# Kernel tuning notes

Measured on AMD Instinct MI355X. Metric: run time of the kernel, lower is better.

Reference implementation:

```python
import jax, jax.numpy as jnp
import numpy as np

B, N, C = 32, 577, 768
H = 12
DH = C // H  # 64
SCALE = DH ** -0.5


def setup_inputs() -> dict:
    key = jax.random.key(0)
    ks = jax.random.split(key, 5)
    x = jax.random.normal(ks[0], (B, N, C), dtype=jnp.float32)
    # Linear params (torch convention: y = x @ W.T + b)
    qkv_w = jax.random.normal(ks[1], (3 * C, C), dtype=jnp.float32) * (C ** -0.5)
    qkv_b = jnp.zeros((3 * C,), dtype=jnp.float32)
    proj_w = jax.random.normal(ks[2], (C, C), dtype=jnp.float32) * (C ** -0.5)
    proj_b = jnp.zeros((C,), dtype=jnp.float32)
    return {"x": x, "qkv_w": qkv_w, "qkv_b": qkv_b, "proj_w": proj_w, "proj_b": proj_b}


def reference(x, qkv_w, qkv_b, proj_w, proj_b):
    b, n, c = x.shape
    qkv = x @ qkv_w.T + qkv_b                       # [B, N, 3C]
    qkv = qkv.reshape(b, n, 3, H, DH).transpose(2, 0, 3, 1, 4)  # [3, B, H, N, DH]
    q, k, v = qkv[0], qkv[1], qkv[2]
    q = q * SCALE
    attn = jnp.einsum('bhnd,bhmd->bhnm', q, k)      # [B, H, N, N]
    # sigmoid -> inverse-sigmoid straight-through rewrite (forward equals logit(sigmoid(attn)))
    sig = jax.nn.sigmoid(attn)
    inv_sig = jnp.log(sig / (1.0 - sig))
    attn_st = attn + jax.lax.stop_gradient(inv_sig - attn)
    p = jax.nn.softmax(attn_st, axis=-1)
    out = jnp.einsum('bhnm,bhmd->bhnd', p, v)       # [B, H, N, DH]
    out = out.transpose(0, 2, 1, 3).reshape(b, n, c)
    return out @ proj_w.T + proj_b
```

## Files before the change

kernel.cpp:

```cpp
#include <hip/hip_runtime.h>

typedef __bf16 bf16;
typedef __attribute__((ext_vector_type(4))) __bf16 bf16x4;
typedef __attribute__((ext_vector_type(8))) __bf16 bf16x8;
typedef __attribute__((ext_vector_type(4))) float f32x4;

#define MFMA_BF16(A_, B_, C_) __builtin_amdgcn_mfma_f32_16x16x32_bf16(A_, B_, C_, 0, 0, 0)

#define BB    32
#define SEQ   577
#define CH    768
#define NH    12
#define DHD   64
#define MROWS (BB * SEQ)
#define NQKV  2304
#define SEQP  584
#define QSCALE 0.1803368801111204f

#define NSTEP 24

__device__ __forceinline__ int xcd_chunk(int bid, int nwg) {
  int q8 = nwg >> 3, r8 = nwg & 7;
  int xcd = bid & 7, sub = bid >> 3;
  return (xcd < r8 ? xcd * (q8 + 1) : r8 * (q8 + 1) + (xcd - r8) * q8) + sub;
}

__device__ __forceinline__ void async_ld16(const bf16* g, bf16* l) {
  __builtin_amdgcn_global_load_lds(
      (const __attribute__((address_space(1))) void*)g,
      (__attribute__((address_space(3))) void*)l, 16, 0, 0);
}

__global__ __launch_bounds__(256) void cvt_bf16(const float* __restrict__ src,
                                                bf16* __restrict__ dst, int n) {
  int idx = (blockIdx.x * 256 + threadIdx.x) * 4;
  if (idx >= n) return;
  float4 v = *(const float4*)(src + idx);
  bf16x4 o = {(bf16)v.x, (bf16)v.y, (bf16)v.z, (bf16)v.w};
  *(bf16x4*)(dst + idx) = o;
}

__global__ __launch_bounds__(256) void pad_v(bf16* __restrict__ vt) {
  int r = blockIdx.x * 256 + threadIdx.x;
  if (r < BB * NH * DHD) {
    bf16* p = vt + (size_t)r * SEQP + SEQ;
#pragma unroll
    for (int i = 0; i < 7; ++i) p[i] = (bf16)0.f;
  }
}

__global__ __launch_bounds__(256, 2)
void gemm_qkv(const bf16* __restrict__ A, const bf16* __restrict__ W,
              const float* __restrict__ bias,
              bf16* __restrict__ qrm, bf16* __restrict__ krm, bf16* __restrict__ vt) {
  __shared__ bf16 As[2][128 * 32];
  __shared__ bf16 Bs[2][128 * 32];
  const int tid = threadIdx.x, lane = tid & 63, wid = tid >> 6;
  const int quad = lane >> 4, r15 = lane & 15;
  const int nbx = (int)gridDim.x;
  const int wg = xcd_chunk((int)blockIdx.y * nbx + (int)blockIdx.x,
                           nbx * (int)gridDim.y);
  const int m0 = (wg / nbx) * 128, n0 = (wg % nbx) * 128;
  const int waveM = wid & 1, waveN = wid >> 1;

  const bf16* aSrc[2];
  const bf16* bSrc[2];
  for (int c = 0; c < 2; ++c) {
    int q = wid * 128 + c * 64 + lane;
    int row = q >> 2;
    int sw = (row ^ (row >> 2)) & 3;
    int kc = (q & 3) ^ sw;
    aSrc[c] = A + (size_t)(m0 + row) * CH + kc * 8;
    bSrc[c] = W + (size_t)(n0 + row) * CH + kc * 8;
  }

  f32x4 acc[4][4];
#pragma unroll
  for (int i = 0; i < 4; ++i)
#pragma unroll
    for (int j = 0; j < 4; ++j) acc[i][j] = (f32x4){0.f, 0.f, 0.f, 0.f};

#define GSTAGE(K0, BUF)                                                   \
  {                                                                       \
    _Pragma("unroll") for (int c = 0; c < 2; ++c) {                       \
      async_ld16(aSrc[c] + (K0), &As[BUF][(wid * 128 + c * 64) * 8]);     \
      async_ld16(bSrc[c] + (K0), &Bs[BUF][(wid * 128 + c * 64) * 8]);     \
    }                                                                     \
  }

#define GCOMPUTE(BUF)                                                     \
  {                                                                       \
    bf16x8 af[4], bfr[4];                                                 \
    _Pragma("unroll") for (int s = 0; s < 4; ++s) {                       \
      int rowA = waveM * 64 + s * 16 + r15;                               \
      int ca = quad ^ ((rowA ^ (rowA >> 2)) & 3);                         \
      af[s] = *(const bf16x8*)(&As[BUF][rowA * 32 + ca * 8]);             \
      int rowB = waveN * 64 + s * 16 + r15;                               \
      int cb = quad ^ ((rowB ^ (rowB >> 2)) & 3);                         \
      bfr[s] = *(const bf16x8*)(&Bs[BUF][rowB * 32 + cb * 8]);            \
    }                                                                     \
    _Pragma("unroll") for (int sm = 0; sm < 4; ++sm)                      \
      _Pragma("unroll") for (int sn = 0; sn < 4; ++sn)                    \
        acc[sm][sn] = MFMA_BF16(af[sm], bfr[sn], acc[sm][sn]);            \
  }

  GSTAGE(0, 0);
  for (int k0 = 0; k0 < CH; k0 += 64) {
    __syncthreads();
    GSTAGE(k0 + 32, 1);
    GCOMPUTE(0);
    __syncthreads();
    if (k0 + 64 < CH) GSTAGE(k0 + 64, 0);
    GCOMPUTE(1);
  }

  int t = (n0 >= 1536) ? 2 : (n0 >= 768 ? 1 : 0);
  if (t < 2) {
#pragma unroll
    for (int sn = 0; sn < 4; ++sn) {
      int gn = n0 + waveN * 64 + sn * 16 + r15;
      float bv = bias[gn];
      int col = gn - t * CH;
#pragma unroll
      for (int sm = 0; sm < 4; ++sm) {
        int gmBase = m0 + waveM * 64 + sm * 16 + quad * 4;
#pragma unroll
        for (int r = 0; r < 4; ++r) {
          int gm = gmBase + r;
          if (gm < MROWS) {
            float v = acc[sm][sn][r] + bv;
            if (t == 0) {
              qrm[(size_t)gm * CH + col] = (bf16)(v * QSCALE);
            } else {
              krm[(size_t)gm * CH + col] = (bf16)v;
            }
          }
        }
      }
    }
  } else {
    bf16* Ld = &Bs[0][0];
#pragma unroll
    for (int p = 0; p < 4; ++p) {
      __syncthreads();
      if (waveN == (p >> 1)) {
        int sn0 = (p & 1) * 2;
#pragma unroll
        for (int s2 = 0; s2 < 2; ++s2) {
          int sn = sn0 + s2;
          int lc = s2 * 16 + r15;
          float bv = bias[n0 + waveN * 64 + sn * 16 + r15];
#pragma unroll
          for (int sm = 0; sm < 4; ++sm)
#pragma unroll
            for (int r = 0; r < 4; ++r) {
              int row = waveM * 64 + sm * 16 + quad * 4 + r;
              Ld[lc * 130 + row] = (bf16)(acc[sm][sn][r] + bv);
            }
        }
      }
      __syncthreads();
#pragma unroll
      for (int cc = 0; cc < 8; ++cc) {
        int c = wid * 8 + cc;
        int gcol = (n0 - 1536) + p * 32 + c;
        int h = gcol >> 6, d = gcol & 63;
#pragma unroll
        for (int it = 0; it < 2; ++it) {
          int row = it * 64 + lane;
          int gm = m0 + row;
          if (gm < MROWS) {
            int b_ = gm / SEQ;
            int n_ = gm - b_ * SEQ;
            vt[((size_t)(b_ * NH + h) * DHD + d) * SEQP + n_] = Ld[c * 130 + row];
          }
        }
      }
    }
  }
}
#undef GSTAGE
#undef GCOMPUTE

__global__ __launch_bounds__(512, 2)
void gemm_proj(const bf16* __restrict__ A, const bf16* __restrict__ W,
               const float* __restrict__ bias, float* __restrict__ out) {
  __shared__ bf16 As[4][256 * 32];
  __shared__ bf16 Bs[4][256 * 32];
  const int tid = threadIdx.x, lane = tid & 63, wid = tid >> 6;
  const int quad = lane >> 4, r15 = lane & 15;

  const int nbx = (int)gridDim.x;
  const int wg = xcd_chunk((int)blockIdx.y * nbx + (int)blockIdx.x,
                           nbx * (int)gridDim.y);
  const int m0 = (wg / nbx) * 256, n0 = (wg % nbx) * 256;

  const int rm = (wid >> 2) * 128;
  const int rn = (wid & 3) * 64;

  int aOff[2], bOff[2];
#pragma unroll
  for (int i = 0; i < 2; ++i) {
    int slot = i * 512 + tid;
    int row = slot >> 2, pc2 = slot & 3;
    int gc2 = pc2 ^ ((row ^ (row >> 2)) & 3);
    aOff[i] = (m0 + row) * CH + gc2 * 8;
    bOff[i] = (n0 + row) * CH + gc2 * 8;
  }

  f32x4 acc[8][4];
#pragma unroll
  for (int i = 0; i < 8; ++i)
#pragma unroll
    for (int j = 0; j < 4; ++j) acc[i][j] = (f32x4){0.f, 0.f, 0.f, 0.f};

#define ISSUE2(S)                                                              \
  {                                                                            \
    const int kb_ = (S) * 32;                                                  \
    const int bf_ = (S) & 3;                                                   \
    _Pragma("unroll") for (int i = 0; i < 2; ++i) {                            \
      async_ld16(A + aOff[i] + kb_, &As[bf_][(i * 512 + tid) * 8]);            \
      async_ld16(W + bOff[i] + kb_, &Bs[bf_][(i * 512 + tid) * 8]);            \
    }                                                                          \
  }

#define COMPUTE2(BF)                                                           \
  {                                                                            \
    bf16x8 bfr[4], afr[8];                                                     \
    _Pragma("unroll") for (int sn = 0; sn < 4; ++sn) {                         \
      int fr = rn + sn * 16 + r15;                                             \
      int pc2 = quad ^ ((fr ^ (fr >> 2)) & 3);                                 \
      bfr[sn] = *(const bf16x8*)(&Bs[BF][fr * 32 + pc2 * 8]);                  \
    }                                                                          \
    _Pragma("unroll") for (int sm = 0; sm < 8; ++sm) {                         \
      int fr = rm + sm * 16 + r15;                                             \
      int pc2 = quad ^ ((fr ^ (fr >> 2)) & 3);                                 \
      afr[sm] = *(const bf16x8*)(&As[BF][fr * 32 + pc2 * 8]);                  \
    }                                                                          \
    _Pragma("unroll") for (int sm = 0; sm < 8; ++sm)                           \
      _Pragma("unroll") for (int sn = 0; sn < 4; ++sn)                         \
        acc[sm][sn] = MFMA_BF16(afr[sm], bfr[sn], acc[sm][sn]);                \
  }

  ISSUE2(0);
  ISSUE2(1);
  for (int s = 0; s < NSTEP; ++s) {
    if (s < NSTEP - 2) {
      ISSUE2(s + 2);
      asm volatile("s_waitcnt vmcnt(8)" ::: "memory");
    } else if (s == NSTEP - 2) {
      asm volatile("s_waitcnt vmcnt(4)" ::: "memory");
    } else {
      asm volatile("s_waitcnt vmcnt(0)" ::: "memory");
    }
    __builtin_amdgcn_s_barrier();
    asm volatile("" ::: "memory");
    COMPUTE2(s & 3);
  }

#pragma unroll
  for (int sn = 0; sn < 4; ++sn) {
    int gn = n0 + rn + sn * 16 + r15;
    float bv = bias[gn];
#pragma unroll
    for (int sm = 0; sm < 8; ++sm) {
      int gmBase = m0 + rm + sm * 16 + quad * 4;
#pragma unroll
      for (int r = 0; r < 4; ++r) {
        int gm = gmBase + r;
        if (gm < MROWS) out[(size_t)gm * CH + gn] = acc[sm][sn][r] + bv;
      }
    }
  }
}
#undef ISSUE2
#undef COMPUTE2

__global__ __launch_bounds__(256, 4)
void attn_kernel(const bf16* __restrict__ qrm, const bf16* __restrict__ krm,
                 const bf16* __restrict__ vt, bf16* __restrict__ ob) {
  __shared__ bf16 Ks[2][64 * 32];
  __shared__ bf16 Vt[2][64 * 32];
  __shared__ bf16 Ps[4][2][16 * 40];
  const int tid = threadIdx.x, lane = tid & 63, wid = tid >> 6;
  const int quad = lane >> 4, r15 = lane & 15;
  const int nbx = (int)gridDim.x;
  const int wg = xcd_chunk((int)blockIdx.y * nbx + (int)blockIdx.x,
                           nbx * (int)gridDim.y);
  const int qt = wg % nbx, bh = wg / nbx;
  const int b_ = bh / NH, h = bh - b_ * NH;
  const bf16* vtb = vt + (size_t)bh * DHD * SEQP;
  const bf16* krmb = krm + (size_t)b_ * SEQ * CH + h * DHD;

  const int hr_ = tid >> 2;
  const int kc_ = (tid & 3) ^ ((hr_ ^ (hr_ >> 2)) & 3);
  const int offK_ = ((hr_ & 1) * 32) + kc_ * 8;
  const bf16* kp_ = krmb + (size_t)(hr_ >> 1) * CH + offK_;
  const bf16* vp_ = vtb + (size_t)hr_ * SEQP + kc_ * 8;

#define ASTAGE_CLEAN(BUF)                                                      \
  {                                                                            \
    async_ld16(kp_, &Ks[BUF][tid * 8]);                                        \
    async_ld16(vp_, &Vt[BUF][tid * 8]);                                        \
    kp_ += 32 * CH;                                                            \
    vp_ += 32;                                                                 \
  }

#define ASTAGE_TAIL(BUF)                                                       \
  {                                                                            \
    async_ld16(krmb + (size_t)(SEQ - 1) * CH + offK_, &Ks[BUF][tid * 8]);      \
    async_ld16(vtb + (size_t)hr_ * SEQP + (SEQ - 1), &Vt[BUF][tid * 8]);       \
  }

  bf16x8 qf[2][2];
#pragma unroll
  for (int g = 0; g < 2; ++g) {
    int qrow = qt * 128 + wid * 32 + g * 16 + r15;
    if (qrow > SEQ - 1) qrow = SEQ - 1;
    const bf16* qp = qrm + (size_t)(b_ * SEQ + qrow) * CH + h * DHD + quad * 8;
    qf[g][0] = *(const bf16x8*)qp;
    qf[g][1] = *(const bf16x8*)(qp + 32);
  }

  bf16x8 ones;
#pragma unroll
  for (int i = 0; i < 8; ++i) ones[i] = (bf16)1.0f;

  f32x4 oacc[2][4];
#pragma unroll
  for (int g = 0; g < 2; ++g)
#pragma unroll
    for (int i = 0; i < 4; ++i) oacc[g][i] = (f32x4){0.f, 0.f, 0.f, 0.f};
  f32x4 sacc0 = (f32x4){0.f, 0.f, 0.f, 0.f};
  f32x4 sacc1 = (f32x4){0.f, 0.f, 0.f, 0.f};

  bf16* P0 = &Ps[wid][0][0];
  bf16* P1 = &Ps[wid][1][0];

#define QKT_PV(BUF, MASKED)                                                    \
  {                                                                            \
    f32x4 s0[2], s1[2];                                                        \
    _Pragma("unroll") for (int sj = 0; sj < 2; ++sj) {                         \
      int hr0 = (sj * 16 + r15) * 2, hr1 = hr0 + 1;                            \
      int p0c = quad ^ ((hr0 ^ (hr0 >> 2)) & 3);                               \
      int p1c = quad ^ ((hr1 ^ (hr1 >> 2)) & 3);                               \
      bf16x8 kf0 = *(const bf16x8*)(&Ks[BUF][hr0 * 32 + p0c * 8]);             \
      bf16x8 kf1 = *(const bf16x8*)(&Ks[BUF][hr1 * 32 + p1c * 8]);             \
      f32x4 z = (f32x4){0.f, 0.f, 0.f, 0.f};                                   \
      s0[sj] = MFMA_BF16(kf0, qf[0][0], z);                                    \
      s0[sj] = MFMA_BF16(kf1, qf[0][1], s0[sj]);                               \
      s1[sj] = MFMA_BF16(kf0, qf[1][0], z);                                    \
      s1[sj] = MFMA_BF16(kf1, qf[1][1], s1[sj]);                               \
    }                                                                          \
    _Pragma("unroll") for (int sj = 0; sj < 2; ++sj)                           \
      _Pragma("unroll") for (int r = 0; r < 4; ++r) {                          \
        if (MASKED) {                                                          \
          bool ok = (sj == 0) && (quad == 0) && (r == 0);     \
          s0[sj][r] = ok ? __builtin_amdgcn_exp2f(s0[sj][r]) : 0.f;            \
          s1[sj][r] = ok ? __builtin_amdgcn_exp2f(s1[sj][r]) : 0.f;            \
        } else {                                                               \
          s0[sj][r] = __builtin_amdgcn_exp2f(s0[sj][r]);                       \
          s1[sj][r] = __builtin_amdgcn_exp2f(s1[sj][r]);                       \
        }                                                                      \
      }                                                                        \
    _Pragma("unroll") for (int sj = 0; sj < 2; ++sj) {                         \
      bf16x4 p0 = {(bf16)s0[sj][0], (bf16)s0[sj][1],                           \
                   (bf16)s0[sj][2], (bf16)s0[sj][3]};                          \
      bf16x4 p1 = {(bf16)s1[sj][0], (bf16)s1[sj][1],                           \
                   (bf16)s1[sj][2], (bf16)s1[sj][3]};                          \
      *(bf16x4*)(P0 + r15 * 40 + sj * 16 + quad * 4) = p0;                     \
      *(bf16x4*)(P1 + r15 * 40 + sj * 16 + quad * 4) = p1;                     \
    }                                                                          \
    asm volatile("s_waitcnt lgkmcnt(0)" ::: "memory");   \
    {                                                                          \
      bf16x8 pf0 = *(const bf16x8*)(P0 + r15 * 40 + quad * 8);                 \
      bf16x8 pf1 = *(const bf16x8*)(P1 + r15 * 40 + quad * 8);                 \
      sacc0 = MFMA_BF16(pf0, ones, sacc0);          \
      sacc1 = MFMA_BF16(pf1, ones, sacc1);                                     \
      _Pragma("unroll") for (int sd = 0; sd < 4; ++sd) {                       \
        int dv = sd * 16 + r15;                                                \
        int pv = quad ^ ((dv ^ (dv >> 2)) & 3);                                \
        bf16x8 vf = *(const bf16x8*)(&Vt[BUF][dv * 32 + pv * 8]);              \
        oacc[0][sd] = MFMA_BF16(pf0, vf, oacc[0][sd]);                         \
        oacc[1][sd] = MFMA_BF16(pf1, vf, oacc[1][sd]);                         \
      }                                                                        \
    }                                                                          \
  }

  ASTAGE_CLEAN(0);
  int buf = 0;
  for (int t = 0; t < 18; ++t) {
    __syncthreads();
    if (t < 17) { ASTAGE_CLEAN(buf ^ 1); } else { ASTAGE_TAIL(buf ^ 1); }
    QKT_PV(buf, 0);
    buf ^= 1;
  }
  __syncthreads();
  QKT_PV(buf, 1);
#undef ASTAGE_CLEAN
#undef ASTAGE_TAIL
#undef QKT_PV

#pragma unroll
  for (int g = 0; g < 2; ++g) {
#pragma unroll
    for (int r = 0; r < 4; ++r) {
      int m = quad * 4 + r;
      float rs = (g == 0) ? sacc0[r] : sacc1[r];
      int orow = qt * 128 + wid * 32 + g * 16 + m;
      if (orow < SEQ) {
        float inv = 1.0f / rs;
        size_t rowoff = ((size_t)(b_ * SEQ + orow)) * CH + h * DHD;
#pragma unroll
        for (int sd = 0; sd < 4; ++sd)
          ob[rowoff + sd * 16 + r15] = (bf16)(oacc[g][sd][r] * inv);
      }
    }
  }
}

extern "C" void kernel_launch(void* const* d_in, const int* in_sizes, int n_in,
                              void* d_out, int out_size, void* d_ws, size_t ws_size,
                              hipStream_t stream) {
  const float* x      = (const float*)d_in[0];
  const float* qkv_w  = (const float*)d_in[1];
  const float* qkv_b  = (const float*)d_in[2];
  const float* proj_w = (const float*)d_in[3];
  const float* proj_b = (const float*)d_in[4];
  float* out = (float*)d_out;

  char* w = (char*)d_ws;
  bf16* xb  = (bf16*)(w);
  bf16* wqp = (bf16*)(w + 28360704);
  bf16* qrm = (bf16*)(w + 31899648);
  bf16* krm = (bf16*)(w + 60260352);
  bf16* vtb = (bf16*)(w + 88621056);

  cvt_bf16<<<(MROWS * CH / 4 + 255) / 256, 256, 0, stream>>>(x, xb, MROWS * CH);
  cvt_bf16<<<(NQKV * CH / 4 + 255) / 256, 256, 0, stream>>>(qkv_w, wqp, NQKV * CH);
  pad_v<<<(BB * NH * DHD + 255) / 256, 256, 0, stream>>>(vtb);

  gemm_qkv<<<dim3(NQKV / 128, 145), 256, 0, stream>>>(
      xb, wqp, qkv_b, qrm, krm, vtb);

  attn_kernel<<<dim3(5, BB * NH), 256, 0, stream>>>(qrm, krm, vtb, xb);

  cvt_bf16<<<(CH * CH / 4 + 255) / 256, 256, 0, stream>>>(proj_w, wqp, CH * CH);

  gemm_proj<<<dim3(CH / 256, 73), 512, 0, stream>>>(xb, wqp, proj_b, out);
}
```

Before: 339.7 us.

## Fuse fp32-to-bf16 conversion of x into QKV GEMM A-tile loading

Drops the separate cvt_bf16 pass over x. The QKV GEMM now reads fp32 x straight into registers, converts it to bf16 and writes it to LDS, prefetching one step ahead. The pipeline is rebuilt around 32-wide K steps with one barrier per step. This saves a full write and reread of the bf16 copy of x. The cost is that every N-tile block rereads x as fp32, which is twice the global bytes per A load across 18 column blocks, and the A path now goes through registers instead of async LDS loads.

```diff
diff --git a/kernel.cpp b/kernel.cpp
--- a/kernel.cpp
+++ b/kernel.cpp
@@ -50,7 +50,7 @@
 }
 
 __global__ __launch_bounds__(256, 2)
-void gemm_qkv(const bf16* __restrict__ A, const bf16* __restrict__ W,
+void gemm_qkv(const float* __restrict__ X, const bf16* __restrict__ W,
               const float* __restrict__ bias,
               bf16* __restrict__ qrm, bf16* __restrict__ krm, bf16* __restrict__ vt) {
   __shared__ bf16 As[2][128 * 32];
@@ -63,15 +63,19 @@
   const int m0 = (wg / nbx) * 128, n0 = (wg % nbx) * 128;
   const int waveM = wid & 1, waveN = wid >> 1;
 
-  const bf16* aSrc[2];
+  const float* aSrcF[2];
   const bf16* bSrc[2];
+  int aSlot[2];
   for (int c = 0; c < 2; ++c) {
     int q = wid * 128 + c * 64 + lane;
     int row = q >> 2;
     int sw = (row ^ (row >> 2)) & 3;
     int kc = (q & 3) ^ sw;
-    aSrc[c] = A + (size_t)(m0 + row) * CH + kc * 8;
+    int grow = m0 + row;
+    if (grow > MROWS - 1) grow = MROWS - 1;
+    aSrcF[c] = X + (size_t)grow * CH + kc * 8;
     bSrc[c] = W + (size_t)(n0 + row) * CH + kc * 8;
+    aSlot[c] = q * 8;
   }
 
   f32x4 acc[4][4];
@@ -80,38 +84,60 @@
 #pragma unroll
     for (int j = 0; j < 4; ++j) acc[i][j] = (f32x4){0.f, 0.f, 0.f, 0.f};
 
-#define GSTAGE(K0, BUF)                                                   \
+  float4 a0lo, a0hi, a1lo, a1hi;
+
+#define LOADA(S)                                                          \
   {                                                                       \
-    _Pragma("unroll") for (int c = 0; c < 2; ++c) {                       \
-      async_ld16(aSrc[c] + (K0), &As[BUF][(wid * 128 + c * 64) * 8]);     \
-      async_ld16(bSrc[c] + (K0), &Bs[BUF][(wid * 128 + c * 64) * 8]);     \
-    }                                                                     \
+    a0lo = *(const float4*)(aSrcF[0] + (S) * 32);                         \
+    a0hi = *(const float4*)(aSrcF[0] + (S) * 32 + 4);                     \
+    a1lo = *(const float4*)(aSrcF[1] + (S) * 32);                         \
+    a1hi = *(const float4*)(aSrcF[1] + (S) * 32 + 4);                     \
+  }
+
+#define DSWRITE_A(BUF)                                                    \
+  {                                                                       \
+    bf16x8 v0 = {(bf16)a0lo.x, (bf16)a0lo.y, (bf16)a0lo.z, (bf16)a0lo.w, \
+                 (bf16)a0hi.x, (bf16)a0hi.y, (bf16)a0hi.z, (bf16)a0hi.w};\
+    bf16x8 v1 = {(bf16)a1lo.x, (bf16)a1lo.y, (bf16)a1lo.z, (bf16)a1lo.w, \
+                 (bf16)a1hi.x, (bf16)a1hi.y, (bf16)a1hi.z, (bf16)a1hi.w};\
+    *(bf16x8*)(&As[BUF][aSlot[0]]) = v0;                                  \
+    *(bf16x8*)(&As[BUF][aSlot[1]]) = v1;                                  \
+  }
+
+#define GSTAGE_B(S, BUF)                                                  \
+  {                                                                       \
+    _Pragma("unroll") for (int c = 0; c < 2; ++c)                         \
+      async_ld16(bSrc[c] + (S) * 32, &Bs[BUF][(wid * 128 + c * 64) * 8]); \
   }
 
 #define GCOMPUTE(BUF)                                                     \
   {                                                                       \
     bf16x8 af[4], bfr[4];                                                 \
-    _Pragma("unroll") for (int s = 0; s < 4; ++s) {                       \
-      int rowA = waveM * 64 + s * 16 + r15;                               \
+    _Pragma("unroll") for (int s_ = 0; s_ < 4; ++s_) {                    \
+      int rowA = waveM * 64 + s_ * 16 + r15;                              \
       int ca = quad ^ ((rowA ^ (rowA >> 2)) & 3);                         \
-      af[s] = *(const bf16x8*)(&As[BUF][rowA * 32 + ca * 8]);             \
-      int rowB = waveN * 64 + s * 16 + r15;                               \
+      af[s_] = *(const bf16x8*)(&As[BUF][rowA * 32 + ca * 8]);            \
+      int rowB = waveN * 64 + s_ * 16 + r15;                              \
       int cb = quad ^ ((rowB ^ (rowB >> 2)) & 3);                         \
-      bfr[s] = *(const bf16x8*)(&Bs[BUF][rowB * 32 + cb * 8]);            \
+      bfr[s_] = *(const bf16x8*)(&Bs[BUF][rowB * 32 + cb * 8]);           \
     }                                                                     \
     _Pragma("unroll") for (int sm = 0; sm < 4; ++sm)                      \
       _Pragma("unroll") for (int sn = 0; sn < 4; ++sn)                    \
         acc[sm][sn] = MFMA_BF16(af[sm], bfr[sn], acc[sm][sn]);            \
   }
 
-  GSTAGE(0, 0);
-  for (int k0 = 0; k0 < CH; k0 += 64) {
+  LOADA(0);
+  DSWRITE_A(0);
+  LOADA(1);
+  GSTAGE_B(0, 0);
+  for (int s = 0; s < NSTEP; ++s) {
     __syncthreads();
-    GSTAGE(k0 + 32, 1);
-    GCOMPUTE(0);
-    __syncthreads();
-    if (k0 + 64 < CH) GSTAGE(k0 + 64, 0);
-    GCOMPUTE(1);
+    if (s < NSTEP - 1) {
+      DSWRITE_A((s + 1) & 1);
+      if (s < NSTEP - 2) LOADA(s + 2);
+      GSTAGE_B(s + 1, (s + 1) & 1);
+    }
+    GCOMPUTE(s & 1);
   }
 
   int t = (n0 >= 1536) ? 2 : (n0 >= 768 ? 1 : 0);
@@ -179,7 +205,9 @@
     }
   }
 }
-#undef GSTAGE
+#undef LOADA
+#undef DSWRITE_A
+#undef GSTAGE_B
 #undef GCOMPUTE
 
 __global__ __launch_bounds__(512, 2)
@@ -436,12 +464,11 @@
   bf16* krm = (bf16*)(w + 60260352);
   bf16* vtb = (bf16*)(w + 88621056);
 
-  cvt_bf16<<<(MROWS * CH / 4 + 255) / 256, 256, 0, stream>>>(x, xb, MROWS * CH);
   cvt_bf16<<<(NQKV * CH / 4 + 255) / 256, 256, 0, stream>>>(qkv_w, wqp, NQKV * CH);
   pad_v<<<(BB * NH * DHD + 255) / 256, 256, 0, stream>>>(vtb);
 
   gemm_qkv<<<dim3(NQKV / 128, 145), 256, 0, stream>>>(
-      xb, wqp, qkv_b, qrm, krm, vtb);
+      x, wqp, qkv_b, qrm, krm, vtb);
 
   attn_kernel<<<dim3(5, BB * NH), 256, 0, stream>>>(qrm, krm, vtb, xb);
 
```

After: 354.4 us. +4.4%, slower.
